# Optimization experiments

Measured on AMD Instinct MI355X. Metric: run time of the kernel, lower is better.

Reference implementation:

```python
import jax, jax.numpy as jnp
import numpy as np

EMB = 512
HEADS = 8
HEAD_DIM = EMB // HEADS
FFN = 2048
RECENCY = 0.05
NEG = -1e9


def setup_inputs() -> dict:
    key = jax.random.key(0)
    ks = jax.random.split(key, 16)
    s = 0.02
    d = {
        'x': jax.random.normal(ks[0], (2, 2048, EMB), jnp.float32),
        'wq': jax.random.normal(ks[1], (EMB, EMB), jnp.float32) * s,
        'bq': jnp.zeros((EMB,), jnp.float32),
        'wk': jax.random.normal(ks[2], (EMB, EMB), jnp.float32) * s,
        'bk': jnp.zeros((EMB,), jnp.float32),
        'wv': jax.random.normal(ks[3], (EMB, EMB), jnp.float32) * s,
        'bv': jnp.zeros((EMB,), jnp.float32),
        'wo': jax.random.normal(ks[4], (EMB, EMB), jnp.float32) * s,
        'bo': jnp.zeros((EMB,), jnp.float32),
        'ln1_g': jnp.ones((EMB,), jnp.float32),
        'ln1_b': jnp.zeros((EMB,), jnp.float32),
        'w1': jax.random.normal(ks[5], (EMB, FFN), jnp.float32) * s,
        'b1': jnp.zeros((FFN,), jnp.float32),
        'w2': jax.random.normal(ks[6], (FFN, EMB), jnp.float32) * s,
        'b2': jnp.zeros((EMB,), jnp.float32),
        'ln2_g': jnp.ones((EMB,), jnp.float32),
        'ln2_b': jnp.zeros((EMB,), jnp.float32),
    }
    return d


def _layernorm(x, g, b, eps=1e-5):
    mu = jnp.mean(x, axis=-1, keepdims=True)
    var = jnp.var(x, axis=-1, keepdims=True)
    return (x - mu) * jax.lax.rsqrt(var + eps) * g + b


def _split_heads(x):
    b, s, _ = x.shape
    return x.reshape(b, s, HEADS, HEAD_DIM).transpose(0, 2, 1, 3)  # [b,h,s,d]


def _block(x, wq, bq, wk, bk, wv, bv, wo, bo, ln1_g, ln1_b, w1, b1, w2, b2, ln2_g, ln2_b):
    b, s, _ = x.shape
    q = _split_heads(x @ wq + bq)
    k = _split_heads(x @ wk + bk)
    v = _split_heads(x @ wv + bv)
    scores = jnp.einsum('bhqd,bhkd->bhqk', q, k) / np.sqrt(HEAD_DIM)
    pos = jnp.arange(s)
    dist = jnp.abs(pos[:, None] - pos[None, :]).astype(scores.dtype)
    bias = -RECENCY * dist  # recency (ALiBi-like) bias
    bias = jnp.where(pos[None, :] > pos[:, None], NEG, bias)  # causal
    scores = scores + bias[None, None]
    attn = jax.nn.softmax(scores, axis=-1)
    ctx = jnp.einsum('bhqk,bhkd->bhqd', attn, v)
    ctx = ctx.transpose(0, 2, 1, 3).reshape(b, s, EMB)
    attn_out = ctx @ wo + bo
    x = _layernorm(x + attn_out, ln1_g, ln1_b)
    ffn = jax.nn.relu(x @ w1 + b1) @ w2 + b2
    x = _layernorm(x + ffn, ln2_g, ln2_b)
    return x


def reference(x, wq, bq, wk, bk, wv, bv, wo, bo, ln1_g, ln1_b, w1, b1, w2, b2, ln2_g, ln2_b):
    return _block(x, wq, bq, wk, bk, wv, bv, wo, bo, ln1_g, ln1_b, w1, b1, w2, b2, ln2_g, ln2_b)
```

## Files before the change

kernel.cpp:

```cpp
#include <hip/hip_runtime.h>
#include <hip/hip_bf16.h>
#include <stdint.h>

using u16 = unsigned short;
using bf16x8 = __attribute__((ext_vector_type(8))) short;
using f32x4  = __attribute__((ext_vector_type(4))) float;

__device__ __forceinline__ u16 f2bf(float f) {
    union { float f; unsigned u; } c; c.f = f;
    unsigned u = c.u;
    return (u16)((u + 0x7fffu + ((u >> 16) & 1u)) >> 16);
}
__device__ __forceinline__ float bf2f(u16 h) {
    union { unsigned u; float f; } c; c.u = ((unsigned)h) << 16;
    return c.f;
}

#define EMB 512
#define SEQ 2048
#define BATCH 2
#define NTOK (BATCH * SEQ)
#define FFN_DIM 2048
#define NEGINF (-1e9f)
#define LOG2E 1.44269504f

__global__ void conv_all(const float* __restrict__ x,
                         const float* __restrict__ wq, const float* __restrict__ wk,
                         const float* __restrict__ wv, const float* __restrict__ bq,
                         const float* __restrict__ bk, const float* __restrict__ bv,
                         const float* __restrict__ wo, const float* __restrict__ w1,
                         const float* __restrict__ w2,
                         u16* __restrict__ xb, u16* __restrict__ wqkv_t,
                         float* __restrict__ bqkv, u16* __restrict__ wo_t,
                         u16* __restrict__ w1_t, u16* __restrict__ w2_t) {
    int i = blockIdx.x * 256 + threadIdx.x;
    if (i < 2097152) {
        xb[i] = f2bf(x[i]);
    } else if (i < 2883584) {
        int idx = i - 2097152;
        int n = idx >> 9, k = idx & 511;
        int sel = n >> 9, nn = n & 511;
        const float* w = (sel == 0) ? wq : (sel == 1) ? wk : wv;
        wqkv_t[idx] = f2bf(w[k * 512 + nn]);
        if (k == 0) {
            const float* b = (sel == 0) ? bq : (sel == 1) ? bk : bv;
            bqkv[n] = b[nn];
        }
    } else if (i < 3145728) {
        int idx = i - 2883584;
        int n = idx >> 9, k = idx & 511;
        wo_t[idx] = f2bf(wo[k * 512 + n]);
    } else if (i < 4194304) {
        int idx = i - 3145728;
        int n = idx >> 9, k = idx & 511;
        w1_t[idx] = f2bf(w1[k * 2048 + n]);
    } else if (i < 5242880) {
        int idx = i - 4194304;
        int n = idx >> 11, k = idx & 2047;
        w2_t[idx] = f2bf(w2[k * 512 + n]);
    }
}

template <int EPI, int BM, int BN>
__global__ __launch_bounds__(256) void gemm_bt(
    const u16* __restrict__ A, const u16* __restrict__ Bt,
    const float* __restrict__ bias, const float* __restrict__ res,
    u16* __restrict__ outb, float* __restrict__ outf, u16* __restrict__ vt_out,
    int M, int N, int K) {
    constexpr int RM = BM / 32, RN = BN / 32 > 0 ? BN / 32 : 1;
    __shared__ __align__(16) u16 a_s[BM * 72];
    __shared__ __align__(16) u16 b_s[BN * 72];
    const int t = threadIdx.x;
    const int wave = t >> 6, lane = t & 63;
    const int wr = wave >> 1, wc = wave & 1;
    const int lr = lane & 15, lh = lane >> 4;
    const int m0 = blockIdx.x * BM, n0 = blockIdx.y * BN;

    f32x4 acc[RM][RN] = {};

    for (int kt = 0; kt < K; kt += 64) {
        __syncthreads();
#pragma unroll
        for (int i = 0; i < BM / 32; ++i) {
            int chunk = t + 256 * i;
            int row = chunk >> 3, c8 = (chunk & 7) * 8;
            *(int4*)&a_s[row * 72 + c8] = *(const int4*)&A[(size_t)(m0 + row) * K + kt + c8];
        }
#pragma unroll
        for (int i = 0; i < (BN + 31) / 32; ++i) {
            int chunk = t + 256 * i;
            int row = chunk >> 3, c8 = (chunk & 7) * 8;
            if (BN >= 32 || chunk < BN * 8)
                *(int4*)&b_s[row * 72 + c8] = *(const int4*)&Bt[(size_t)(n0 + row) * K + kt + c8];
        }
        __syncthreads();
#pragma unroll
        for (int ks = 0; ks < 64; ks += 32) {
            bf16x8 af[RM], bfr[RN];
#pragma unroll
            for (int m = 0; m < RM; ++m)
                af[m] = *(const bf16x8*)&a_s[(wr * (BM / 2) + m * 16 + lr) * 72 + ks + lh * 8];
#pragma unroll
            for (int n = 0; n < RN; ++n)
                bfr[n] = *(const bf16x8*)&b_s[(wc * (BN / 2) + n * 16 + lr) * 72 + ks + lh * 8];
#pragma unroll
            for (int m = 0; m < RM; ++m)
#pragma unroll
                for (int n = 0; n < RN; ++n)
                    acc[m][n] = __builtin_amdgcn_mfma_f32_16x16x32_bf16(af[m], bfr[n], acc[m][n], 0, 0, 0);
        }
    }

#pragma unroll
    for (int m = 0; m < RM; ++m) {
        int row = m0 + wr * (BM / 2) + m * 16 + lh * 4;
#pragma unroll
        for (int n = 0; n < RN; ++n) {
            int col = n0 + wc * (BN / 2) + n * 16 + lr;
            float bv = bias[col];
            if (EPI == 3 && col >= 1024) {
                int dg = col - 1024, hh = dg >> 6, dd = dg & 63;
                int bb = row >> 11, ss = row & 2047;
                ushort4 pk;
                pk.x = f2bf(acc[m][n][0] + bv);
                pk.y = f2bf(acc[m][n][1] + bv);
                pk.z = f2bf(acc[m][n][2] + bv);
                pk.w = f2bf(acc[m][n][3] + bv);
                *(ushort4*)&vt_out[((size_t)((bb * 8 + hh) * 64 + dd)) * SEQ + ss] = pk;
            } else {
#pragma unroll
                for (int r = 0; r < 4; ++r) {
                    float v = acc[m][n][r] + bv;
                    size_t o = (size_t)(row + r) * N + col;
                    if (EPI == 1) outb[o] = f2bf(v > 0.f ? v : 0.f);
                    else if (EPI == 2) outf[o] = v + res[o];
                    else outb[o] = f2bf(v);
                }
            }
        }
    }
}

__global__ __launch_bounds__(256) void attn_part(
    const u16* __restrict__ qkv, const u16* __restrict__ vt,
    u16* __restrict__ opart, float* __restrict__ lpart) {
    const int bid = blockIdx.x;
    const int xcd = bid & 7, j = bid >> 3;
    const int bh = 2 * xcd + (j & 1);
    const int qt = 127 - (j >> 1);
    const int b = bh >> 3, h = bh & 7;
    const int w = threadIdx.x >> 6, lane = threadIdx.x & 63;
    const int lr = lane & 15, lh = lane >> 4;
    __shared__ __align__(16) u16 p_all[4][16 * 72];
    u16* p_lds = p_all[w];

    const int q0 = qt * 16;
    const int nt = (q0 + 15) / 64 + 1;
    const int clen = (nt + 3) >> 2;
    const int k0 = w * clen;
    const int k1 = (k0 + clen < nt) ? (k0 + clen) : nt;

    const size_t qbase = (size_t)(b * SEQ + q0 + lr) * 1536 + h * 64;
    bf16x8 aq0 = *(const bf16x8*)&qkv[qbase + lh * 8];
    bf16x8 aq1 = *(const bf16x8*)&qkv[qbase + 32 + lh * 8];

    const float SC = 0.125f * LOG2E;
    const float RC = 0.05f * LOG2E;

    f32x4 acc_o[4] = {};
    float tsum[4] = {0.f, 0.f, 0.f, 0.f};

    for (int kt = k0; kt < k1; ++kt) {
        f32x4 s[4];
#pragma unroll
        for (int n = 0; n < 4; ++n) {
            int kcol = kt * 64 + n * 16 + lr;
            size_t kbase = (size_t)(b * SEQ + kcol) * 1536 + 512 + h * 64;
            bf16x8 bk0 = *(const bf16x8*)&qkv[kbase + lh * 8];
            bf16x8 bk1 = *(const bf16x8*)&qkv[kbase + 32 + lh * 8];
            f32x4 z = {};
            z = __builtin_amdgcn_mfma_f32_16x16x32_bf16(aq0, bk0, z, 0, 0, 0);
            s[n] = __builtin_amdgcn_mfma_f32_16x16x32_bf16(aq1, bk1, z, 0, 0, 0);
        }
        if (kt == nt - 1) {
#pragma unroll
            for (int n = 0; n < 4; ++n) {
                int k = kt * 64 + n * 16 + lr;
#pragma unroll
                for (int r = 0; r < 4; ++r) {
                    int q = q0 + lh * 4 + r;
                    float v = s[n][r] * SC + ((k > q) ? NEGINF : -RC * (float)(q - k));
                    float p = exp2f(v);
                    tsum[r] += p;
                    p_lds[(lh * 4 + r) * 72 + n * 16 + lr] = f2bf(p);
                }
            }
        } else {
#pragma unroll
            for (int n = 0; n < 4; ++n) {
                int k = kt * 64 + n * 16 + lr;
#pragma unroll
                for (int r = 0; r < 4; ++r) {
                    int q = q0 + lh * 4 + r;
                    float p = exp2f(s[n][r] * SC - RC * (float)(q - k));
                    tsum[r] += p;
                    p_lds[(lh * 4 + r) * 72 + n * 16 + lr] = f2bf(p);
                }
            }
        }
#pragma unroll
        for (int ks = 0; ks < 2; ++ks) {
            bf16x8 pa = *(const bf16x8*)&p_lds[lr * 72 + ks * 32 + lh * 8];
#pragma unroll
            for (int nd = 0; nd < 4; ++nd) {
                size_t vrow = (size_t)(bh * 64 + nd * 16 + lr) * SEQ + kt * 64 + ks * 32 + lh * 8;
                bf16x8 bv = *(const bf16x8*)&vt[vrow];
                acc_o[nd] = __builtin_amdgcn_mfma_f32_16x16x32_bf16(pa, bv, acc_o[nd], 0, 0, 0);
            }
        }
    }

#pragma unroll
    for (int msk = 1; msk < 16; msk <<= 1)
#pragma unroll
        for (int r = 0; r < 4; ++r) tsum[r] += __shfl_xor(tsum[r], msk);

    const int idx = (w * 128 + qt) * 16 + bh;
    u16* ob = opart + (size_t)idx * 1024;
#pragma unroll
    for (int nd = 0; nd < 4; ++nd) {
        ushort4 pk;
        pk.x = f2bf(acc_o[nd][0]); pk.y = f2bf(acc_o[nd][1]);
        pk.z = f2bf(acc_o[nd][2]); pk.w = f2bf(acc_o[nd][3]);
        *(ushort4*)&ob[(nd * 16 + lr) * 16 + lh * 4] = pk;
    }
    if (lr == 0) {
#pragma unroll
        for (int r = 0; r < 4; ++r)
            lpart[idx * 16 + lh * 4 + r] = tsum[r];
    }
}

__global__ __launch_bounds__(256) void attn_merge(
    const u16* __restrict__ opart, const float* __restrict__ lpart, u16* __restrict__ ctx) {
    const int bid = blockIdx.x;
    const int xcd = bid & 7, j = bid >> 3;
    const int bh = 2 * xcd + (j & 1);
    const int qt = j >> 1;
    const int b = bh >> 3, h = bh & 7;
    __shared__ __align__(16) u16 o_lds[4][1024];
    __shared__ float l_lds[64];
    const int t = threadIdx.x;
#pragma unroll
    for (int c = 0; c < 4; ++c) {
        const int idx = (c * 128 + qt) * 16 + bh;
        ((ushort4*)o_lds[c])[t] = ((const ushort4*)(opart + (size_t)idx * 1024))[t];
    }
    if (t < 64) {
        int c = t >> 4, row = t & 15;
        int idx = (c * 128 + qt) * 16 + bh;
        l_lds[t] = lpart[idx * 16 + row];
    }
    __syncthreads();
#pragma unroll
    for (int i = 0; i < 4; ++i) {
        int e = t + 256 * i;
        int row = e >> 6, col = e & 63;
        float den = l_lds[row] + l_lds[16 + row] + l_lds[32 + row] + l_lds[48 + row];
        float num = bf2f(o_lds[0][col * 16 + row]) + bf2f(o_lds[1][col * 16 + row])
                  + bf2f(o_lds[2][col * 16 + row]) + bf2f(o_lds[3][col * 16 + row]);
        ctx[(size_t)(b * SEQ + qt * 16 + row) * EMB + h * 64 + col] = f2bf(num / den);
    }
}

template <bool WRITE_BF>
__global__ __launch_bounds__(256) void lnorm(
    const float* __restrict__ in, const float* __restrict__ g, const float* __restrict__ bta,
    float* __restrict__ outf, u16* __restrict__ outb) {
    const int row = blockIdx.x * 4 + (threadIdx.x >> 6);
    const int lane = threadIdx.x & 63;
    const float* p = in + (size_t)row * EMB;
    float4 v0 = ((const float4*)p)[lane];
    float4 v1 = ((const float4*)p)[64 + lane];
    float sum = v0.x + v0.y + v0.z + v0.w + v1.x + v1.y + v1.z + v1.w;
    float sq = v0.x*v0.x + v0.y*v0.y + v0.z*v0.z + v0.w*v0.w
             + v1.x*v1.x + v1.y*v1.y + v1.z*v1.z + v1.w*v1.w;
#pragma unroll
    for (int msk = 1; msk < 64; msk <<= 1) {
        sum += __shfl_xor(sum, msk);
        sq  += __shfl_xor(sq, msk);
    }
    float mu = sum * (1.f / EMB);
    float var = sq * (1.f / EMB) - mu * mu;
    float rs = rsqrtf(var + 1e-5f);
    float4 g0 = ((const float4*)g)[lane], g1 = ((const float4*)g)[64 + lane];
    float4 b0 = ((const float4*)bta)[lane], b1 = ((const float4*)bta)[64 + lane];
    float o0x = (v0.x - mu) * rs * g0.x + b0.x;
    float o0y = (v0.y - mu) * rs * g0.y + b0.y;
    float o0z = (v0.z - mu) * rs * g0.z + b0.z;
    float o0w = (v0.w - mu) * rs * g0.w + b0.w;
    float o1x = (v1.x - mu) * rs * g1.x + b1.x;
    float o1y = (v1.y - mu) * rs * g1.y + b1.y;
    float o1z = (v1.z - mu) * rs * g1.z + b1.z;
    float o1w = (v1.w - mu) * rs * g1.w + b1.w;
    float4* po = (float4*)(outf + (size_t)row * EMB);
    po[lane] = make_float4(o0x, o0y, o0z, o0w);
    po[64 + lane] = make_float4(o1x, o1y, o1z, o1w);
    if (WRITE_BF) {
        u16* pb = outb + (size_t)row * EMB;
        int c = lane * 4;
        pb[c] = f2bf(o0x); pb[c + 1] = f2bf(o0y); pb[c + 2] = f2bf(o0z); pb[c + 3] = f2bf(o0w);
        pb[256 + c] = f2bf(o1x); pb[256 + c + 1] = f2bf(o1y);
        pb[256 + c + 2] = f2bf(o1z); pb[256 + c + 3] = f2bf(o1w);
    }
}

extern "C" void kernel_launch(void* const* d_in, const int* in_sizes, int n_in,
                              void* d_out, int out_size, void* d_ws, size_t ws_size,
                              hipStream_t stream) {
    const float* x     = (const float*)d_in[0];
    const float* wq    = (const float*)d_in[1];
    const float* bq    = (const float*)d_in[2];
    const float* wk    = (const float*)d_in[3];
    const float* bk    = (const float*)d_in[4];
    const float* wv    = (const float*)d_in[5];
    const float* bv    = (const float*)d_in[6];
    const float* wo    = (const float*)d_in[7];
    const float* bo    = (const float*)d_in[8];
    const float* ln1_g = (const float*)d_in[9];
    const float* ln1_b = (const float*)d_in[10];
    const float* w1    = (const float*)d_in[11];
    const float* b1    = (const float*)d_in[12];
    const float* w2    = (const float*)d_in[13];
    const float* b2    = (const float*)d_in[14];
    const float* ln2_g = (const float*)d_in[15];
    const float* ln2_b = (const float*)d_in[16];
    float* out = (float*)d_out;

    char* w = (char*)d_ws;
    size_t off = 0;
    auto nxt = [&](size_t bytes) -> void* {
        void* p = w + off;
        off = (off + bytes + 255) & ~(size_t)255;
        return p;
    };
    u16*   xb      = (u16*)nxt((size_t)NTOK * EMB * 2);
    u16*   wqkv_t  = (u16*)nxt((size_t)1536 * 512 * 2);
    float* bqkv    = (float*)nxt(1536 * 4);
    u16*   wo_t    = (u16*)nxt((size_t)512 * 512 * 2);
    u16*   w1_t    = (u16*)nxt((size_t)2048 * 512 * 2);
    u16*   w2_t    = (u16*)nxt((size_t)512 * 2048 * 2);
    u16*   qkvb    = (u16*)nxt((size_t)NTOK * 1536 * 2);
    u16*   vt      = (u16*)nxt((size_t)16 * 64 * SEQ * 2);
    u16*   ctxb    = (u16*)nxt((size_t)NTOK * EMB * 2);
    float* ybuf    = (float*)nxt((size_t)NTOK * EMB * 4);
    float* x1      = (float*)nxt((size_t)NTOK * EMB * 4);
    u16*   x1b     = (u16*)nxt((size_t)NTOK * EMB * 2);
    u16*   hb      = (u16*)nxt((size_t)NTOK * FFN_DIM * 2);

    u16*   opart = (u16*)ybuf;
    float* lpart = (float*)((char*)ybuf + 16777216);

    conv_all<<<20480, 256, 0, stream>>>(x, wq, wk, wv, bq, bk, bv, wo, w1, w2,
                                        xb, wqkv_t, bqkv, wo_t, w1_t, w2_t);

    gemm_bt<3, 64, 64><<<dim3(64, 24), 256, 0, stream>>>(
        xb, wqkv_t, bqkv, nullptr, qkvb, nullptr, vt, NTOK, 1536, 512);
    attn_part<<<2048, 256, 0, stream>>>(qkvb, vt, opart, lpart);
    attn_merge<<<2048, 256, 0, stream>>>(opart, lpart, ctxb);
    gemm_bt<2, 64, 32><<<dim3(64, 16), 256, 0, stream>>>(
        ctxb, wo_t, bo, x, nullptr, ybuf, nullptr, NTOK, 512, 512);
    lnorm<true><<<NTOK / 4, 256, 0, stream>>>(ybuf, ln1_g, ln1_b, x1, x1b);
    gemm_bt<1, 64, 64><<<dim3(64, 32), 256, 0, stream>>>(
        x1b, w1_t, b1, nullptr, hb, nullptr, nullptr, NTOK, FFN_DIM, 512);
    gemm_bt<2, 64, 32><<<dim3(64, 16), 256, 0, stream>>>(
        hb, w2_t, b2, x1, nullptr, ybuf, nullptr, NTOK, EMB, FFN_DIM);
    lnorm<false><<<NTOK / 4, 256, 0, stream>>>(ybuf, ln2_g, ln2_b, out, nullptr);
}
```

Baseline: 270.1 us.

## Fuse attention split-K and merge into one kernel with LDS-shared K/V tiles

Replaces the two-kernel attention (per-wave key-range split writing partial outputs, then a merge kernel) with one fused kernel. Each block now covers 64 queries, four waves of 16 rows each, and walks all causal key tiles. K and V tiles are staged in double-buffered LDS and shared by the four waves, with register prefetch of the next tile. This removes the partial-result round trip through global memory and the extra launch, and cuts redundant global K/V loads. In exchange the grid drops from 2048 to 512 blocks with causal load imbalance, there is a per-tile block barrier, and the final ctx stores are scalar and strided.

```diff
diff --git a/kernel.cpp b/kernel.cpp
--- a/kernel.cpp
+++ b/kernel.cpp
@@ -10,10 +10,6 @@
     union { float f; unsigned u; } c; c.f = f;
     unsigned u = c.u;
     return (u16)((u + 0x7fffu + ((u >> 16) & 1u)) >> 16);
-}
-__device__ __forceinline__ float bf2f(u16 h) {
-    union { unsigned u; float f; } c; c.u = ((unsigned)h) << 16;
-    return c.f;
 }
 
 #define EMB 512
@@ -141,24 +137,24 @@
     }
 }
 
-__global__ __launch_bounds__(256) void attn_part(
-    const u16* __restrict__ qkv, const u16* __restrict__ vt,
-    u16* __restrict__ opart, float* __restrict__ lpart) {
+__global__ __launch_bounds__(256) void attn_fused(
+    const u16* __restrict__ qkv, const u16* __restrict__ vt, u16* __restrict__ ctx) {
     const int bid = blockIdx.x;
     const int xcd = bid & 7, j = bid >> 3;
     const int bh = 2 * xcd + (j & 1);
-    const int qt = 127 - (j >> 1);
+    const int qb = 31 - (j >> 1);
     const int b = bh >> 3, h = bh & 7;
-    const int w = threadIdx.x >> 6, lane = threadIdx.x & 63;
+    const int t = threadIdx.x;
+    const int w = t >> 6, lane = t & 63;
     const int lr = lane & 15, lh = lane >> 4;
+
+    __shared__ __align__(16) u16 k_s[2][64 * 72];
+    __shared__ __align__(16) u16 v_s[2][64 * 72];
     __shared__ __align__(16) u16 p_all[4][16 * 72];
     u16* p_lds = p_all[w];
 
-    const int q0 = qt * 16;
-    const int nt = (q0 + 15) / 64 + 1;
-    const int clen = (nt + 3) >> 2;
-    const int k0 = w * clen;
-    const int k1 = (k0 + clen < nt) ? (k0 + clen) : nt;
+    const int nt = qb + 1;
+    const int q0 = qb * 64 + w * 16;
 
     const size_t qbase = (size_t)(b * SEQ + q0 + lr) * 1536 + h * 64;
     bf16x8 aq0 = *(const bf16x8*)&qkv[qbase + lh * 8];
@@ -167,17 +163,37 @@
     const float SC = 0.125f * LOG2E;
     const float RC = 0.05f * LOG2E;
 
+#pragma unroll
+    for (int i = 0; i < 2; ++i) {
+        int u = t + 256 * i;
+        int row = u >> 3, ch = u & 7;
+        *(int4*)&k_s[0][row * 72 + ch * 8] =
+            *(const int4*)&qkv[(size_t)(b * SEQ + row) * 1536 + 512 + h * 64 + ch * 8];
+        *(int4*)&v_s[0][row * 72 + ch * 8] =
+            *(const int4*)&vt[(size_t)(bh * 64 + row) * SEQ + ch * 8];
+    }
+    __syncthreads();
+
     f32x4 acc_o[4] = {};
     float tsum[4] = {0.f, 0.f, 0.f, 0.f};
-
-    for (int kt = k0; kt < k1; ++kt) {
+    int cur = 0;
+
+    for (int kt = 0; kt < nt; ++kt) {
+        int4 kreg[2], vreg[2];
+        if (kt + 1 < nt) {
+#pragma unroll
+            for (int i = 0; i < 2; ++i) {
+                int u = t + 256 * i;
+                int row = u >> 3, ch = u & 7;
+                kreg[i] = *(const int4*)&qkv[(size_t)(b * SEQ + (kt + 1) * 64 + row) * 1536 + 512 + h * 64 + ch * 8];
+                vreg[i] = *(const int4*)&vt[(size_t)(bh * 64 + row) * SEQ + (kt + 1) * 64 + ch * 8];
+            }
+        }
         f32x4 s[4];
 #pragma unroll
         for (int n = 0; n < 4; ++n) {
-            int kcol = kt * 64 + n * 16 + lr;
-            size_t kbase = (size_t)(b * SEQ + kcol) * 1536 + 512 + h * 64;
-            bf16x8 bk0 = *(const bf16x8*)&qkv[kbase + lh * 8];
-            bf16x8 bk1 = *(const bf16x8*)&qkv[kbase + 32 + lh * 8];
+            bf16x8 bk0 = *(const bf16x8*)&k_s[cur][(n * 16 + lr) * 72 + lh * 8];
+            bf16x8 bk1 = *(const bf16x8*)&k_s[cur][(n * 16 + lr) * 72 + 32 + lh * 8];
             f32x4 z = {};
             z = __builtin_amdgcn_mfma_f32_16x16x32_bf16(aq0, bk0, z, 0, 0, 0);
             s[n] = __builtin_amdgcn_mfma_f32_16x16x32_bf16(aq1, bk1, z, 0, 0, 0);
@@ -213,11 +229,21 @@
             bf16x8 pa = *(const bf16x8*)&p_lds[lr * 72 + ks * 32 + lh * 8];
 #pragma unroll
             for (int nd = 0; nd < 4; ++nd) {
-                size_t vrow = (size_t)(bh * 64 + nd * 16 + lr) * SEQ + kt * 64 + ks * 32 + lh * 8;
-                bf16x8 bv = *(const bf16x8*)&vt[vrow];
+                bf16x8 bv = *(const bf16x8*)&v_s[cur][(nd * 16 + lr) * 72 + ks * 32 + lh * 8];
                 acc_o[nd] = __builtin_amdgcn_mfma_f32_16x16x32_bf16(pa, bv, acc_o[nd], 0, 0, 0);
             }
         }
+        if (kt + 1 < nt) {
+#pragma unroll
+            for (int i = 0; i < 2; ++i) {
+                int u = t + 256 * i;
+                int row = u >> 3, ch = u & 7;
+                *(int4*)&k_s[cur ^ 1][row * 72 + ch * 8] = kreg[i];
+                *(int4*)&v_s[cur ^ 1][row * 72 + ch * 8] = vreg[i];
+            }
+            cur ^= 1;
+        }
+        __syncthreads();
     }
 
 #pragma unroll
@@ -225,52 +251,13 @@
 #pragma unroll
         for (int r = 0; r < 4; ++r) tsum[r] += __shfl_xor(tsum[r], msk);
 
-    const int idx = (w * 128 + qt) * 16 + bh;
-    u16* ob = opart + (size_t)idx * 1024;
-#pragma unroll
-    for (int nd = 0; nd < 4; ++nd) {
-        ushort4 pk;
-        pk.x = f2bf(acc_o[nd][0]); pk.y = f2bf(acc_o[nd][1]);
-        pk.z = f2bf(acc_o[nd][2]); pk.w = f2bf(acc_o[nd][3]);
-        *(ushort4*)&ob[(nd * 16 + lr) * 16 + lh * 4] = pk;
-    }
-    if (lr == 0) {
-#pragma unroll
-        for (int r = 0; r < 4; ++r)
-            lpart[idx * 16 + lh * 4 + r] = tsum[r];
-    }
-}
-
-__global__ __launch_bounds__(256) void attn_merge(
-    const u16* __restrict__ opart, const float* __restrict__ lpart, u16* __restrict__ ctx) {
-    const int bid = blockIdx.x;
-    const int xcd = bid & 7, j = bid >> 3;
-    const int bh = 2 * xcd + (j & 1);
-    const int qt = j >> 1;
-    const int b = bh >> 3, h = bh & 7;
-    __shared__ __align__(16) u16 o_lds[4][1024];
-    __shared__ float l_lds[64];
-    const int t = threadIdx.x;
-#pragma unroll
-    for (int c = 0; c < 4; ++c) {
-        const int idx = (c * 128 + qt) * 16 + bh;
-        ((ushort4*)o_lds[c])[t] = ((const ushort4*)(opart + (size_t)idx * 1024))[t];
-    }
-    if (t < 64) {
-        int c = t >> 4, row = t & 15;
-        int idx = (c * 128 + qt) * 16 + bh;
-        l_lds[t] = lpart[idx * 16 + row];
-    }
-    __syncthreads();
-#pragma unroll
-    for (int i = 0; i < 4; ++i) {
-        int e = t + 256 * i;
-        int row = e >> 6, col = e & 63;
-        float den = l_lds[row] + l_lds[16 + row] + l_lds[32 + row] + l_lds[48 + row];
-        float num = bf2f(o_lds[0][col * 16 + row]) + bf2f(o_lds[1][col * 16 + row])
-                  + bf2f(o_lds[2][col * 16 + row]) + bf2f(o_lds[3][col * 16 + row]);
-        ctx[(size_t)(b * SEQ + qt * 16 + row) * EMB + h * 64 + col] = f2bf(num / den);
-    }
+#pragma unroll
+    for (int nd = 0; nd < 4; ++nd)
+#pragma unroll
+        for (int r = 0; r < 4; ++r) {
+            size_t o = (size_t)(b * SEQ + q0 + lh * 4 + r) * EMB + h * 64 + nd * 16 + lr;
+            ctx[o] = f2bf(acc_o[nd][r] / tsum[r]);
+        }
 }
 
 template <bool WRITE_BF>
@@ -358,16 +345,12 @@
     u16*   x1b     = (u16*)nxt((size_t)NTOK * EMB * 2);
     u16*   hb      = (u16*)nxt((size_t)NTOK * FFN_DIM * 2);
 
-    u16*   opart = (u16*)ybuf;
-    float* lpart = (float*)((char*)ybuf + 16777216);
-
     conv_all<<<20480, 256, 0, stream>>>(x, wq, wk, wv, bq, bk, bv, wo, w1, w2,
                                         xb, wqkv_t, bqkv, wo_t, w1_t, w2_t);
 
     gemm_bt<3, 64, 64><<<dim3(64, 24), 256, 0, stream>>>(
         xb, wqkv_t, bqkv, nullptr, qkvb, nullptr, vt, NTOK, 1536, 512);
-    attn_part<<<2048, 256, 0, stream>>>(qkvb, vt, opart, lpart);
-    attn_merge<<<2048, 256, 0, stream>>>(opart, lpart, ctxb);
+    attn_fused<<<512, 256, 0, stream>>>(qkvb, vt, ctxb);
     gemm_bt<2, 64, 32><<<dim3(64, 16), 256, 0, stream>>>(
         ctxb, wo_t, bo, x, nullptr, ybuf, nullptr, NTOK, 512, 512);
     lnorm<true><<<NTOK / 4, 256, 0, stream>>>(ybuf, ln1_g, ln1_b, x1, x1b);
```

Result: slower. 283.6 us (+5.0%).

## Load GEMM tiles directly into LDS via global_load_lds and enlarge tiles

Applied to the files above, without the earlier changes.

The GEMM kernel now stages A and B tiles with direct global-to-LDS loads, so the data no longer passes through registers. The padded 72-element LDS rows become unpadded 64-element rows, which the direct-load layout requires. Tile shapes change to 128x64 for the QKV and FFN1 GEMMs and 64x64 for the output-projection and FFN2 GEMMs, which reduces the grid sizes. Dropping the padding may bring LDS bank conflicts on the fragment reads, and the larger tiles mean fewer blocks per GEMM.

```diff
diff --git a/kernel.cpp b/kernel.cpp
--- a/kernel.cpp
+++ b/kernel.cpp
@@ -14,6 +14,12 @@
 __device__ __forceinline__ float bf2f(u16 h) {
     union { unsigned u; float f; } c; c.u = ((unsigned)h) << 16;
     return c.f;
+}
+
+__device__ __forceinline__ void gl_lds16(const u16* g, u16* l) {
+    __builtin_amdgcn_global_load_lds(
+        (__attribute__((address_space(1))) void*)(g),
+        (__attribute__((address_space(3))) void*)(l), 16, 0, 0);
 }
 
 #define EMB 512
@@ -62,47 +68,43 @@
 }
 
 template <int EPI, int BM, int BN>
-__global__ __launch_bounds__(256) void gemm_bt(
+__global__ __launch_bounds__(256) void gemm_ld(
     const u16* __restrict__ A, const u16* __restrict__ Bt,
     const float* __restrict__ bias, const float* __restrict__ res,
     u16* __restrict__ outb, float* __restrict__ outf, u16* __restrict__ vt_out,
     int M, int N, int K) {
-    constexpr int RM = BM / 32, RN = BN / 32 > 0 ? BN / 32 : 1;
-    __shared__ __align__(16) u16 a_s[BM * 72];
-    __shared__ __align__(16) u16 b_s[BN * 72];
+    constexpr int RM = BM / 32, RN = BN / 32;
+    __shared__ __align__(16) u16 a_s[BM * 64];
+    __shared__ __align__(16) u16 b_s[BN * 64];
     const int t = threadIdx.x;
     const int wave = t >> 6, lane = t & 63;
     const int wr = wave >> 1, wc = wave & 1;
     const int lr = lane & 15, lh = lane >> 4;
     const int m0 = blockIdx.x * BM, n0 = blockIdx.y * BN;
+    const int grow = lane >> 3, gcol = (lane & 7) * 8;
 
     f32x4 acc[RM][RN] = {};
 
     for (int kt = 0; kt < K; kt += 64) {
         __syncthreads();
 #pragma unroll
-        for (int i = 0; i < BM / 32; ++i) {
-            int chunk = t + 256 * i;
-            int row = chunk >> 3, c8 = (chunk & 7) * 8;
-            *(int4*)&a_s[row * 72 + c8] = *(const int4*)&A[(size_t)(m0 + row) * K + kt + c8];
-        }
-#pragma unroll
-        for (int i = 0; i < (BN + 31) / 32; ++i) {
-            int chunk = t + 256 * i;
-            int row = chunk >> 3, c8 = (chunk & 7) * 8;
-            if (BN >= 32 || chunk < BN * 8)
-                *(int4*)&b_s[row * 72 + c8] = *(const int4*)&Bt[(size_t)(n0 + row) * K + kt + c8];
-        }
+        for (int i = 0; i < BM / 32; ++i)
+            gl_lds16(&A[(size_t)(m0 + i * 32 + wave * 8 + grow) * K + kt + gcol],
+                     &a_s[i * 2048 + wave * 512]);
+#pragma unroll
+        for (int i = 0; i < BN / 32; ++i)
+            gl_lds16(&Bt[(size_t)(n0 + i * 32 + wave * 8 + grow) * K + kt + gcol],
+                     &b_s[i * 2048 + wave * 512]);
         __syncthreads();
 #pragma unroll
         for (int ks = 0; ks < 64; ks += 32) {
             bf16x8 af[RM], bfr[RN];
 #pragma unroll
             for (int m = 0; m < RM; ++m)
-                af[m] = *(const bf16x8*)&a_s[(wr * (BM / 2) + m * 16 + lr) * 72 + ks + lh * 8];
+                af[m] = *(const bf16x8*)&a_s[(wr * (BM / 2) + m * 16 + lr) * 64 + ks + lh * 8];
 #pragma unroll
             for (int n = 0; n < RN; ++n)
-                bfr[n] = *(const bf16x8*)&b_s[(wc * (BN / 2) + n * 16 + lr) * 72 + ks + lh * 8];
+                bfr[n] = *(const bf16x8*)&b_s[(wc * (BN / 2) + n * 16 + lr) * 64 + ks + lh * 8];
 #pragma unroll
             for (int m = 0; m < RM; ++m)
 #pragma unroll
@@ -364,16 +366,16 @@
     conv_all<<<20480, 256, 0, stream>>>(x, wq, wk, wv, bq, bk, bv, wo, w1, w2,
                                         xb, wqkv_t, bqkv, wo_t, w1_t, w2_t);
 
-    gemm_bt<3, 64, 64><<<dim3(64, 24), 256, 0, stream>>>(
+    gemm_ld<3, 128, 64><<<dim3(32, 24), 256, 0, stream>>>(
         xb, wqkv_t, bqkv, nullptr, qkvb, nullptr, vt, NTOK, 1536, 512);
     attn_part<<<2048, 256, 0, stream>>>(qkvb, vt, opart, lpart);
     attn_merge<<<2048, 256, 0, stream>>>(opart, lpart, ctxb);
-    gemm_bt<2, 64, 32><<<dim3(64, 16), 256, 0, stream>>>(
+    gemm_ld<2, 64, 64><<<dim3(64, 8), 256, 0, stream>>>(
         ctxb, wo_t, bo, x, nullptr, ybuf, nullptr, NTOK, 512, 512);
     lnorm<true><<<NTOK / 4, 256, 0, stream>>>(ybuf, ln1_g, ln1_b, x1, x1b);
-    gemm_bt<1, 64, 64><<<dim3(64, 32), 256, 0, stream>>>(
+    gemm_ld<1, 128, 64><<<dim3(32, 32), 256, 0, stream>>>(
         x1b, w1_t, b1, nullptr, hb, nullptr, nullptr, NTOK, FFN_DIM, 512);
-    gemm_bt<2, 64, 32><<<dim3(64, 16), 256, 0, stream>>>(
+    gemm_ld<2, 64, 64><<<dim3(64, 8), 256, 0, stream>>>(
         hb, w2_t, b2, x1, nullptr, ybuf, nullptr, NTOK, EMB, FFN_DIM);
     lnorm<false><<<NTOK / 4, 256, 0, stream>>>(ybuf, ln2_g, ln2_b, out, nullptr);
 }
```

After: 264.9 us. About the same (-1.9%).
